# Optimization experiments

Measured on AMD Instinct MI355X. Metric: run time of the kernel, lower is better.

## Reference

```python
import jax, jax.numpy as jnp
import numpy as np

N, F, E, WID, M, K = 100000, 128, 128, 4, 25000, 16
HID = WID * F    # width * num_features = 512
DHID = WID * E   # discriminator hidden = 512
EPS = 1e-5


def _v2v(x, v_idx, w_e):
    """Hypergraph v2v mean aggregation: v->e mean (scaled by w_e), then e->v mean."""
    Mm, Kk = v_idx.shape
    C = x.shape[1]
    ef = jnp.zeros((Mm, C), x.dtype)
    for k in range(Kk):  # K is small and static; avoids a [M,K,C] materialization
        ef = ef + x[v_idx[:, k]]
    ef = ef * (w_e / Kk)[:, None]  # weighted edge features [M, C]
    out = jnp.zeros_like(x)
    deg = jnp.zeros((x.shape[0],), x.dtype)
    for k in range(Kk):
        out = out.at[v_idx[:, k]].add(ef)
        deg = deg.at[v_idx[:, k]].add(1.0)
    return out / jnp.maximum(deg, 1.0)[:, None]


def _bn(h, g, bt):
    # BatchNorm1d in training mode: biased batch stats over vertex dim
    m = h.mean(0)
    v = ((h - m) ** 2).mean(0)
    return g * (h - m) * jax.lax.rsqrt(v + EPS) + bt


def _conv(x, Wt, b, g, bt, v_idx, w_e, last=False):
    h = _bn(x @ Wt.T + b, g, bt)
    h = _v2v(h, v_idx, w_e)
    return h if last else jax.nn.relu(h)  # dropout = identity (eval mode)


def setup_inputs() -> dict:
    key = jax.random.key(0)
    ks = iter(jax.random.split(key, 64))

    def lin(o, i):
        s = 1.0 / np.sqrt(i)
        return (jax.random.uniform(next(ks), (o, i), minval=-s, maxval=s, dtype=jnp.float32),
                jax.random.uniform(next(ks), (o,), minval=-s, maxval=s, dtype=jnp.float32))

    d = {}
    d["X"] = jax.random.normal(next(ks), (N, F), dtype=jnp.float32)
    d["v_idx"] = jax.random.randint(next(ks), (M, K), 0, N, dtype=jnp.int32)
    d["w_e"] = jax.random.uniform(next(ks), (M,), dtype=jnp.float32)
    for name, (o, i) in [("enc1", (HID, F)), ("enc2", (E, HID)), ("fc", (E, HID)),
                         ("f1u", (E, E)), ("f2u", (E, E)), ("f1r", (E, E)), ("f2r", (E, E)),
                         ("f1", (E, E)), ("f2", (E, E)),
                         ("dis1", (DHID, E)), ("dis2", (2, DHID)),
                         ("dec1", (HID, E)), ("dec2", (F, HID))]:
        Wt, b = lin(o, i)
        d[name + "_W"] = Wt
        d[name + "_b"] = b
    for name, c in [("enc1", HID), ("enc2", E), ("dis1", DHID), ("dis2", 2), ("dec1", HID), ("dec2", F)]:
        d[name + "_g"] = jnp.ones((c,), jnp.float32)
        d[name + "_bt"] = jnp.zeros((c,), jnp.float32)
    return d


def reference(X, v_idx, w_e,
              enc1_W, enc1_b, enc2_W, enc2_b, fc_W, fc_b,
              f1u_W, f1u_b, f2u_W, f2u_b, f1r_W, f1r_b, f2r_W, f2r_b,
              f1_W, f1_b, f2_W, f2_b,
              dis1_W, dis1_b, dis2_W, dis2_b, dec1_W, dec1_b, dec2_W, dec2_b,
              enc1_g, enc1_bt, enc2_g, enc2_bt, dis1_g, dis1_bt, dis2_g, dis2_bt,
              dec1_g, dec1_bt, dec2_g, dec2_bt):
    # encoder (returns last output and first-layer output)
    x1 = _conv(X, enc1_W, enc1_b, enc1_g, enc1_bt, v_idx, w_e)            # [N, HID]
    xe = _conv(x1, enc2_W, enc2_b, enc2_g, enc2_bt, v_idx, w_e, last=True)  # [N, E]
    xe1 = x1 @ fc_W.T + fc_b                                               # [N, E]
    # GRU-style gating
    z = jax.nn.sigmoid(xe1 @ f1u_W.T + f1u_b + xe @ f2u_W.T + f2u_b)
    r = jax.nn.sigmoid(xe1 @ f1r_W.T + f1r_b + xe @ f2r_W.T + f2r_b)
    o = jnp.tanh(xe1 @ f1_W.T + f1_b + (r * xe) @ f2_W.T + f2_b)
    outs = z * o + (1.0 - z) * xe                                          # [N, E]
    # attention pooling (n = input_size - 1)
    dd = (outs - outs.mean(0)) ** 2
    vv = dd.sum(0) / (N - 1)
    ee = dd / (4.0 * (vv + 0.001)) + 0.5
    proto = (outs * jax.nn.sigmoid(ee)).sum(0)                             # [E]
    # gradient reversal is identity in the forward pass
    h = _conv(outs, dis1_W, dis1_b, dis1_g, dis1_bt, v_idx, w_e)
    xdis = _conv(h, dis2_W, dis2_b, dis2_g, dis2_bt, v_idx, w_e, last=True)  # [N, 2]
    h = _conv(outs, dec1_W, dec1_b, dec1_g, dec1_bt, v_idx, w_e)
    x_de = _conv(h, dec2_W, dec2_b, dec2_g, dec2_bt, v_idx, w_e, last=True)  # [N, F]
    return (outs, x_de, proto, xdis)
```

## Files before the change

### kernel.cpp

```cpp
#include <hip/hip_runtime.h>
#include <cstddef>
#include <cstdint>

static constexpr int NV = 100000;
static constexpr int NP = 100096;
static constexpr int ME = 25000;
static constexpr int MEP = 25088;
static constexpr int KE = 16;
static constexpr float BN_EPS = 1e-5f;

typedef unsigned int u32;
typedef __attribute__((ext_vector_type(8))) short s16x8;
typedef __attribute__((ext_vector_type(8))) unsigned short u16x8;
typedef __attribute__((ext_vector_type(4))) float f32x4;

__device__ __forceinline__ float sigm(float x) { return 1.0f / (1.0f + expf(-x)); }
__device__ __forceinline__ float bf2f(unsigned short u) {
    union { u32 i; float f; } v; v.i = ((u32)u) << 16; return v.f;
}
__device__ __forceinline__ unsigned short f2bf(float f) {
    union { float f; u32 i; } v; v.f = f;
    u32 u = v.i;
    return (unsigned short)((u + 0x7FFFu + ((u >> 16) & 1u)) >> 16);
}

#define GLD16(g, l) __builtin_amdgcn_global_load_lds(                          \
    (__attribute__((address_space(1))) const unsigned int*)(g),                \
    (__attribute__((address_space(3))) unsigned int*)(l), 16, 0, 0)

#define STAGE_A(b, k0)                                                         \
  {                                                                            \
    unsigned short* sA_ = sm + (b) * 8192;                                     \
    _Pragma("unroll")                                                          \
    for (int i_ = 0; i_ < 4; ++i_) {                                           \
      const unsigned short* g_ = A + (size_t)(bm + 32 * w + 8 * i_ + (l >> 3)) * IC + (k0) + swz; \
      GLD16(g_, sA_ + 2048 * w + 512 * i_);                                    \
    }                                                                          \
  }

__global__ __launch_bounds__(256)
void mfma_gemm(const unsigned short* __restrict__ A, int IC,
               const unsigned short* __restrict__ W, const float* __restrict__ bias,
               unsigned short* __restrict__ Cb, int ldb, int cb0,
               unsigned short* __restrict__ Cb2, int ldb2, int splitN,
               float* __restrict__ s1f, float* __restrict__ s2f, int statsC)
{
    __shared__ unsigned short sm[2 * 8192];
    const int bm = blockIdx.y * 128;
    const int bn = blockIdx.x * 64;
    const int tid = threadIdx.x;
    const int l = tid & 63, w = tid >> 6;
    const int wrow = w >> 1, wcol = w & 1;

    f32x4 acc[4][2];
    #pragma unroll
    for (int m = 0; m < 4; ++m)
        #pragma unroll
        for (int n = 0; n < 2; ++n)
            #pragma unroll
            for (int r = 0; r < 4; ++r) acc[m][n][r] = 0.f;

    const int swz = (((l & 7) ^ (l >> 3)) << 3);
    const int nt = IC >> 6;

    STAGE_A(0, 0);
    asm volatile("s_waitcnt vmcnt(0)" ::: "memory");
    __builtin_amdgcn_s_barrier();

    for (int t = 0; t < nt; ++t) {
        const int cur = t & 1;
        if (t + 1 < nt) STAGE_A(cur ^ 1, (t + 1) << 6);
        const unsigned short* sA = sm + cur * 8192;
        #pragma unroll
        for (int ks = 0; ks < 2; ++ks) {
            const int koff = ks * 32 + ((l >> 4) << 3);
            s16x8 afr[4], bfr[2];
            #pragma unroll
            for (int m = 0; m < 4; ++m) {
                int row = wrow * 64 + m * 16 + (l & 15);
                afr[m] = *(const s16x8*)&sA[row * 64 + (koff ^ ((l & 7) << 3))];
            }
            #pragma unroll
            for (int n = 0; n < 2; ++n) {
                int col = bn + wcol * 32 + n * 16 + (l & 15);
                bfr[n] = *(const s16x8*)&W[(size_t)col * IC + (t << 6) + koff];
            }
            #pragma unroll
            for (int m = 0; m < 4; ++m)
                #pragma unroll
                for (int n = 0; n < 2; ++n)
                    acc[m][n] = __builtin_amdgcn_mfma_f32_16x16x32_bf16(
                        afr[m], bfr[n], acc[m][n], 0, 0, 0);
        }
        asm volatile("s_waitcnt vmcnt(0)" ::: "memory");
        __builtin_amdgcn_s_barrier();
    }

    unsigned short* dst = Cb;
    int ld = ldb, co = cb0;
    if (Cb2 && bn >= splitN) { dst = Cb2; ld = ldb2; co = -splitN; }

    #pragma unroll
    for (int n = 0; n < 2; ++n) {
        const int col = bn + wcol * 32 + n * 16 + (l & 15);
        const float bs = bias[col];
        float ssum = 0.f, sq = 0.f;
        #pragma unroll
        for (int m = 0; m < 4; ++m) {
            const int row0 = bm + wrow * 64 + m * 16 + ((l >> 4) << 2);
            #pragma unroll
            for (int r = 0; r < 4; ++r) {
                float v = acc[m][n][r] + bs;
                int row = row0 + r;
                if (dst) dst[(size_t)row * ld + co + col] = f2bf(v);
                if (s1f && col < statsC && row < NV) { ssum += v; sq += v * v; }
            }
        }
        if (s1f && col < statsC) {
            ssum += __shfl_xor(ssum, 16); ssum += __shfl_xor(ssum, 32);
            sq   += __shfl_xor(sq, 16);   sq   += __shfl_xor(sq, 32);
            if ((l >> 4) == 0) {
                atomicAdd(&s1f[col], ssum);
                atomicAdd(&s2f[col], sq);
            }
        }
    }
}

__global__ __launch_bounds__(256)
void mfma_gemm_vtx2(const unsigned short* __restrict__ A,
                    const unsigned short* __restrict__ W,
                    const float* __restrict__ P, const float* __restrict__ Q,
                    const float* __restrict__ sw,
                    unsigned short* __restrict__ dst, int ldd, int colStart,
                    int disCols, const unsigned short* __restrict__ disW,
                    float2* __restrict__ pre22p)
{
    const int IC = 128;
    __shared__ unsigned short sm[2 * 8192];
    const int bm = blockIdx.y * 128;
    const int bx = blockIdx.x;
    const int bn0 = bx * 128;
    const int tid = threadIdx.x;
    const int l = tid & 63, w = tid >> 6;
    const int wrow = w >> 1, wcol = w & 1;

    f32x4 acc[4][4];
    #pragma unroll
    for (int m = 0; m < 4; ++m)
        #pragma unroll
        for (int n = 0; n < 4; ++n)
            #pragma unroll
            for (int r = 0; r < 4; ++r) acc[m][n][r] = 0.f;

    const int swz = (((l & 7) ^ (l >> 3)) << 3);

    STAGE_A(0, 0);
    asm volatile("s_waitcnt vmcnt(0)" ::: "memory");
    __builtin_amdgcn_s_barrier();

    #pragma unroll
    for (int t = 0; t < 2; ++t) {
        const int cur = t & 1;
        if (t == 0) STAGE_A(1, 64);
        const unsigned short* sA = sm + cur * 8192;
        #pragma unroll
        for (int ks = 0; ks < 2; ++ks) {
            const int koff = ks * 32 + ((l >> 4) << 3);
            s16x8 afr[4], bfr[4];
            #pragma unroll
            for (int m = 0; m < 4; ++m) {
                int row = wrow * 64 + m * 16 + (l & 15);
                afr[m] = *(const s16x8*)&sA[row * 64 + (koff ^ ((l & 7) << 3))];
            }
            #pragma unroll
            for (int n = 0; n < 4; ++n) {
                int colg = bn0 + wcol * 64 + n * 16 + (l & 15);
                bfr[n] = *(const s16x8*)&W[(size_t)colg * 128 + (t << 6) + koff];
            }
            #pragma unroll
            for (int m = 0; m < 4; ++m)
                #pragma unroll
                for (int n = 0; n < 4; ++n)
                    acc[m][n] = __builtin_amdgcn_mfma_f32_16x16x32_bf16(
                        afr[m], bfr[n], acc[m][n], 0, 0, 0);
        }
        asm volatile("s_waitcnt vmcnt(0)" ::: "memory");
        __builtin_amdgcn_s_barrier();
    }

    if (bn0 < disCols) {
        float pc[4], qc[4], w0f[4], w1f[4];
        #pragma unroll
        for (int n = 0; n < 4; ++n) {
            int colg = bn0 + wcol * 64 + n * 16 + (l & 15);
            pc[n] = P[colg]; qc[n] = Q[colg];
            w0f[n] = bf2f(disW[colg]);
            w1f[n] = bf2f(disW[512 + colg]);
        }
        const int slice = bx * 2 + wcol;
        #pragma unroll
        for (int m = 0; m < 4; ++m) {
            const int row0 = bm + wrow * 64 + m * 16 + ((l >> 4) << 2);
            #pragma unroll
            for (int r = 0; r < 4; ++r) {
                const int row = row0 + r;
                const float swr = sw[row];
                float p0 = 0.f, p1 = 0.f;
                #pragma unroll
                for (int n = 0; n < 4; ++n) {
                    float h = fmaxf(pc[n] * acc[m][n][r] + swr * qc[n], 0.f);
                    p0 += h * w0f[n];
                    p1 += h * w1f[n];
                }
                p0 += __shfl_xor(p0, 1); p0 += __shfl_xor(p0, 2);
                p0 += __shfl_xor(p0, 4); p0 += __shfl_xor(p0, 8);
                p1 += __shfl_xor(p1, 1); p1 += __shfl_xor(p1, 2);
                p1 += __shfl_xor(p1, 4); p1 += __shfl_xor(p1, 8);
                if ((l & 15) == 0)
                    pre22p[(size_t)slice * NP + row] = make_float2(p0, p1);
            }
        }
    } else {
        #pragma unroll
        for (int n = 0; n < 4; ++n) {
            const int colg = bn0 + wcol * 64 + n * 16 + (l & 15);
            const float pc = P[colg], qc = Q[colg];
            #pragma unroll
            for (int m = 0; m < 4; ++m) {
                const int row0 = bm + wrow * 64 + m * 16 + ((l >> 4) << 2);
                #pragma unroll
                for (int r = 0; r < 4; ++r) {
                    const int row = row0 + r;
                    float h = fmaxf(pc * acc[m][n][r] + sw[row] * qc, 0.f);
                    dst[(size_t)row * ldd + colg - colStart] = f2bf(h);
                }
            }
        }
    }
}

__global__ void reduce22(const float2* __restrict__ p, float* __restrict__ pre22)
{
    int v = blockIdx.x * 256 + threadIdx.x;
    if (v >= NV) return;
    float a = 0.f, b = 0.f;
    #pragma unroll
    for (int s = 0; s < 8; ++s) {
        float2 t = p[(size_t)s * NP + v];
        a += t.x; b += t.y;
    }
    pre22[2 * v] = a;
    pre22[2 * v + 1] = b;
}

__global__ __launch_bounds__(256)
void cov_kernel(const unsigned short* __restrict__ A, float* __restrict__ cov)
{
    __shared__ unsigned short T[128 * 64];
    const int tid = threadIdx.x;
    const int l = tid & 63, w = tid >> 6;

    f32x4 acc[2][8];
    #pragma unroll
    for (int m = 0; m < 2; ++m)
        #pragma unroll
        for (int n = 0; n < 8; ++n)
            #pragma unroll
            for (int r = 0; r < 4; ++r) acc[m][n][r] = 0.f;

    const int r0 = blockIdx.x * 1024;
    for (int ch = 0; ch < 16; ++ch) {
        const int rbase = r0 + ch * 64;
        __syncthreads();
        #pragma unroll
        for (int q = 0; q < 4; ++q) {
            int idx = tid + q * 256;
            int r = idx & 63, cg = idx >> 6;
            int row = rbase + r;
            u16x8 u = {0, 0, 0, 0, 0, 0, 0, 0};
            if (row < NV) u = *(const u16x8*)&A[(size_t)row * 128 + cg * 8];
            #pragma unroll
            for (int j = 0; j < 8; ++j) {
                int c = cg * 8 + j;
                T[c * 64 + (r ^ ((c & 7) << 3))] = u[j];
            }
        }
        __syncthreads();
        #pragma unroll
        for (int ks = 0; ks < 2; ++ks) {
            const int koff = ks * 32 + ((l >> 4) << 3);
            s16x8 fi[2], fj[8];
            #pragma unroll
            for (int m = 0; m < 2; ++m) {
                int c = (w * 2 + m) * 16 + (l & 15);
                fi[m] = *(const s16x8*)&T[c * 64 + (koff ^ ((c & 7) << 3))];
            }
            #pragma unroll
            for (int n = 0; n < 8; ++n) {
                int c = n * 16 + (l & 15);
                fj[n] = *(const s16x8*)&T[c * 64 + (koff ^ ((c & 7) << 3))];
            }
            #pragma unroll
            for (int m = 0; m < 2; ++m)
                #pragma unroll
                for (int n = 0; n < 8; ++n)
                    acc[m][n] = __builtin_amdgcn_mfma_f32_16x16x32_bf16(
                        fi[m], fj[n], acc[m][n], 0, 0, 0);
        }
    }
    #pragma unroll
    for (int m = 0; m < 2; ++m) {
        #pragma unroll
        for (int n = 0; n < 8; ++n) {
            #pragma unroll
            for (int r = 0; r < 4; ++r) {
                int row = (w * 2 + m) * 16 + ((l >> 4) << 2) + r;
                int col = n * 16 + (l & 15);
                atomicAdd(&cov[row * 128 + col], acc[m][n][r]);
            }
        }
    }
}

__global__ __launch_bounds__(128)
void quadform_kernel(const float* __restrict__ cov, const float* __restrict__ colsum,
                     const unsigned short* __restrict__ Wt, const float* __restrict__ bias,
                     float* __restrict__ s1, float* __restrict__ s2)
{
    const int c = blockIdx.x, i = threadIdx.x;
    __shared__ float wv[128];
    __shared__ float red[128][2];
    float wi = bf2f(Wt[c * 128 + i]);
    wv[i] = wi;
    __syncthreads();
    const float* crow = cov + i * 128;
    float dot = 0.f;
    #pragma unroll 8
    for (int j = 0; j < 128; ++j) dot += crow[j] * wv[j];
    red[i][0] = wi * dot;
    red[i][1] = wi * colsum[i];
    __syncthreads();
    for (int s = 64; s > 0; s >>= 1) {
        if (i < s) { red[i][0] += red[i + s][0]; red[i][1] += red[i + s][1]; }
        __syncthreads();
    }
    if (i == 0) {
        float b = bias[c];
        float ws = red[0][1];
        s1[c] = ws + (float)NV * b;
        s2[c] = red[0][0] + 2.f * b * ws + (float)NV * b * b;
    }
}

__global__ void prep_weights(const float* e1, const float* e2, const float* fcw,
                             const float* d1, const float* dc1, const float* dc2,
                             const float* ds2,
                             const float* f1u, const float* f2u,
                             const float* f1r, const float* f2r,
                             const float* f1, const float* f2,
                             const float* f1ub, const float* f2ub,
                             const float* f1rb, const float* f2rb,
                             const float* f1b, const float* f2b,
                             const float* ds1b, const float* dc1b,
                             const float* e2b, const float* fcb,
                             unsigned short* WB, float* bzr, float* bo,
                             float* bdd, float* bef)
{
    int i = blockIdx.x * 256 + threadIdx.x;
    if (i < 65536)           WB[i] = f2bf(e1[i]);
    else if (i < 131072)     WB[i] = f2bf(e2[i - 65536]);
    else if (i < 196608)     WB[i] = f2bf(fcw[i - 131072]);
    else if (i < 262144)     WB[i] = f2bf(d1[i - 196608]);
    else if (i < 327680)     WB[i] = f2bf(dc1[i - 262144]);
    else if (i < 393216)     WB[i] = f2bf(dc2[i - 327680]);
    else if (i < 394240)     WB[i] = f2bf(ds2[i - 393216]);
    else if (i < 459776) {
        int j = i - 394240, row = j >> 8, c = j & 255;
        float v;
        if (row < 128) v = (c < 128) ? f1u[row * 128 + c] : f2u[row * 128 + c - 128];
        else { int rr = row - 128; v = (c < 128) ? f1r[rr * 128 + c] : f2r[rr * 128 + c - 128]; }
        WB[i] = f2bf(v);
    } else if (i < 492544) {
        int j = i - 459776, row = j >> 8, c = j & 255;
        float v = (c < 128) ? f1[row * 128 + c] : f2[row * 128 + c - 128];
        WB[i] = f2bf(v);
    } else if (i < 492800) {
        int o = i - 492544;
        bzr[o] = (o < 128) ? (f1ub[o] + f2ub[o]) : (f1rb[o - 128] + f2rb[o - 128]);
    } else if (i < 492928) {
        int o = i - 492800;
        bo[o] = f1b[o] + f2b[o];
    } else if (i < 493952) {
        int o = i - 492928;
        bdd[o] = (o < 512) ? ds1b[o] : dc1b[o - 512];
    } else if (i < 494208) {
        int o = i - 493952;
        bef[o] = (o < 128) ? e2b[o] : fcb[o - 128];
    }
}

__global__ void cvt_f32_bf16(const float* __restrict__ in, unsigned short* __restrict__ out, int n)
{
    int i = (blockIdx.x * 256 + threadIdx.x) * 4;
    if (i < n) {
        float4 v = *reinterpret_cast<const float4*>(&in[i]);
        out[i] = f2bf(v.x); out[i + 1] = f2bf(v.y);
        out[i + 2] = f2bf(v.z); out[i + 3] = f2bf(v.w);
    }
}

__global__ void bn_finalize_kernel(const float* __restrict__ s1, const float* __restrict__ s2,
                                   const float* __restrict__ g, const float* __restrict__ bt,
                                   float* __restrict__ scale, float* __restrict__ shift,
                                   int C, float invN)
{
    int c = threadIdx.x;
    if (c < C) {
        float m = s1[c] * invN;
        float v = fmaxf(s2[c] * invN - m * m, 0.f);
        float sc = g[c] * rsqrtf(v + BN_EPS);
        scale[c] = sc;
        shift[c] = bt[c] - m * sc;
    }
}

__global__ void bn_finalize_pq(const float* __restrict__ s1, const float* __restrict__ s2,
                               const float* __restrict__ g, const float* __restrict__ bt,
                               const float* __restrict__ bias,
                               float* __restrict__ P, float* __restrict__ Q,
                               int C, int off, float invN)
{
    int c = threadIdx.x;
    if (c < C) {
        int cc = off + c;
        float m = s1[cc] * invN;
        float v = fmaxf(s2[cc] * invN - m * m, 0.f);
        float sc = g[c] * rsqrtf(v + BN_EPS);
        float sh = bt[c] - m * sc;
        P[cc] = sc;
        Q[cc] = sc * bias[c] + sh;
    }
}

__global__ __launch_bounds__(256)
void edge_gather_sum(const unsigned short* __restrict__ x, const int* __restrict__ vidx,
                     unsigned short* __restrict__ ge)
{
    const int e = blockIdx.x * 16 + (threadIdx.x >> 4);
    const int cp = (threadIdx.x & 15) << 3;
    if (e >= ME) return;
    float s[8] = {};
    const int* vi = vidx + e * KE;
    #pragma unroll
    for (int k = 0; k < KE; ++k) {
        int v = vi[k];
        u16x8 u = *(const u16x8*)&x[(size_t)v * 128 + cp];
        #pragma unroll
        for (int j = 0; j < 8; ++j) s[j] += bf2f(u[j]);
    }
    u16x8 o;
    #pragma unroll
    for (int j = 0; j < 8; ++j) o[j] = f2bf(s[j]);
    *(u16x8*)&ge[(size_t)e * 128 + cp] = o;
}

__global__ __launch_bounds__(256)
void csr_gather_g2(const unsigned short* __restrict__ ge, const float* __restrict__ we,
                   const int* __restrict__ rowptr, const int* __restrict__ csr,
                   unsigned short* __restrict__ g2, float* __restrict__ swv)
{
    const int v = blockIdx.x * 16 + (threadIdx.x >> 4);
    const int lg = threadIdx.x & 15;
    if (v >= NP) return;
    if (v >= NV) {
        u16x8 z = {0, 0, 0, 0, 0, 0, 0, 0};
        *(u16x8*)&g2[(size_t)v * 128 + lg * 8] = z;
        if (swv && lg == 0) swv[v] = 0.f;
        return;
    }
    const int s = rowptr[v], e = rowptr[v + 1];
    float a[8] = {};
    float ws = 0.f;
    for (int i = s; i < e; ++i) {
        int ed = csr[i];
        float wt = we[ed];
        ws += wt;
        u16x8 u = *(const u16x8*)&ge[(size_t)ed * 128 + lg * 8];
        #pragma unroll
        for (int j = 0; j < 8; ++j) a[j] = fmaf(wt, bf2f(u[j]), a[j]);
    }
    float inv = 1.0f / (float)max(e - s, 1);
    float invK = inv * (1.0f / KE);
    u16x8 o;
    #pragma unroll
    for (int j = 0; j < 8; ++j) o[j] = f2bf(a[j] * invK);
    *(u16x8*)&g2[(size_t)v * 128 + lg * 8] = o;
    if (swv && lg == 0) swv[v] = ws * inv;
}

__global__ __launch_bounds__(256)
void edge_gather_bf(const unsigned short* __restrict__ pre, const int* __restrict__ vidx,
                    const float* __restrict__ we, const float* __restrict__ scl,
                    const float* __restrict__ shf, unsigned short* __restrict__ ef, int C)
{
    const int tpe = C >> 3;
    const int epb = 256 / tpe;
    const int e = blockIdx.x * epb + threadIdx.x / tpe;
    const int cp = (threadIdx.x % tpe) << 3;
    if (e >= ME) return;
    float s[8] = {};
    const int* vi = vidx + e * KE;
    #pragma unroll
    for (int k = 0; k < KE; ++k) {
        int v = vi[k];
        u16x8 u = *(const u16x8*)&pre[(size_t)v * C + cp];
        #pragma unroll
        for (int j = 0; j < 8; ++j) s[j] += bf2f(u[j]);
    }
    float wv = we[e] * (1.0f / KE);
    u16x8 o;
    #pragma unroll
    for (int j = 0; j < 8; ++j)
        o[j] = f2bf(wv * (scl[cp + j] * s[j] + (float)KE * shf[cp + j]));
    *(u16x8*)&ef[(size_t)e * C + cp] = o;
}

__global__ void edge_gather2_kernel(const float* __restrict__ X, const int* __restrict__ vidx,
                                    const float* __restrict__ we, const float* __restrict__ scale,
                                    const float* __restrict__ shift, float* __restrict__ ef)
{
    int e = blockIdx.x * blockDim.x + threadIdx.x;
    if (e >= ME) return;
    float s0 = 0.f, s1v = 0.f;
    #pragma unroll
    for (int k = 0; k < KE; ++k) {
        int v = vidx[e * KE + k];
        s0 += X[2 * v];
        s1v += X[2 * v + 1];
    }
    float w = we[e] * (1.0f / KE);
    ef[2 * e]     = w * (scale[0] * s0 + (float)KE * shift[0]);
    ef[2 * e + 1] = w * (scale[1] * s1v + (float)KE * shift[1]);
}

__global__ void deg_kernel(const int* __restrict__ vidx, int* __restrict__ deg)
{
    int i = blockIdx.x * blockDim.x + threadIdx.x;
    if (i < ME * KE) atomicAdd(&deg[vidx[i]], 1);
}

__global__ void scan_block_kernel(const int* __restrict__ deg, int* __restrict__ rowptr,
                                  int* __restrict__ blocksums, int n)
{
    __shared__ int tmp[256];
    int i = blockIdx.x * 256 + threadIdx.x;
    int v = (i < n) ? deg[i] : 0;
    tmp[threadIdx.x] = v;
    __syncthreads();
    for (int off = 1; off < 256; off <<= 1) {
        int t = (threadIdx.x >= off) ? tmp[threadIdx.x - off] : 0;
        __syncthreads();
        tmp[threadIdx.x] += t;
        __syncthreads();
    }
    if (i < n) rowptr[i] = tmp[threadIdx.x] - v;
    if (threadIdx.x == 255) blocksums[blockIdx.x] = tmp[255];
}

__global__ void scan_sums_par(int* __restrict__ bs, int nb)
{
    __shared__ int tmp[512];
    int t = threadIdx.x;
    int v = (t < nb) ? bs[t] : 0;
    tmp[t] = v;
    __syncthreads();
    for (int off = 1; off < 512; off <<= 1) {
        int u = (t >= off) ? tmp[t - off] : 0;
        __syncthreads();
        tmp[t] += u;
        __syncthreads();
    }
    if (t < nb) bs[t] = tmp[t] - v;
}

__global__ void scan_add_kernel(int* __restrict__ rowptr, const int* __restrict__ blocksums, int n)
{
    int i = blockIdx.x * 256 + threadIdx.x;
    if (i < n) rowptr[i] += blocksums[blockIdx.x];
    if (i == 0) rowptr[n] = ME * KE;
}

__global__ void csr_fill_kernel(const int* __restrict__ vidx, int* __restrict__ cursor,
                                int* __restrict__ csr)
{
    int i = blockIdx.x * blockDim.x + threadIdx.x;
    if (i < ME * KE) {
        int v = vidx[i];
        int pos = atomicAdd(&cursor[v], 1);
        csr[pos] = i >> 4;
    }
}

__global__ __launch_bounds__(256)
void csr_gather_bf(const unsigned short* __restrict__ ef, int ldE, int cb0E,
                   const int* __restrict__ rowptr, const int* __restrict__ csr,
                   float* __restrict__ outf, int ldf,
                   unsigned short* __restrict__ outb, int ldb, int cb0,
                   unsigned short* __restrict__ outb2, int ldb2,
                   int C, int relu)
{
    const int lpv = C >> 3;
    const int vpb = 256 / lpv;
    const int v = blockIdx.x * vpb + threadIdx.x / lpv;
    const int lg = threadIdx.x % lpv;
    if (v >= NV) return;
    const int s = rowptr[v], e = rowptr[v + 1];
    float a[8] = {};
    int i = s;
    for (; i + 2 <= e; i += 2) {
        int e0 = csr[i], e1 = csr[i + 1];
        u16x8 u0 = *(const u16x8*)&ef[(size_t)e0 * ldE + cb0E + lg * 8];
        u16x8 u1 = *(const u16x8*)&ef[(size_t)e1 * ldE + cb0E + lg * 8];
        #pragma unroll
        for (int j = 0; j < 8; ++j) a[j] += bf2f(u0[j]) + bf2f(u1[j]);
    }
    if (i < e) {
        int e0 = csr[i];
        u16x8 u0 = *(const u16x8*)&ef[(size_t)e0 * ldE + cb0E + lg * 8];
        #pragma unroll
        for (int j = 0; j < 8; ++j) a[j] += bf2f(u0[j]);
    }
    float inv = 1.0f / (float)max(e - s, 1);
    #pragma unroll
    for (int j = 0; j < 8; ++j) {
        float x = a[j] * inv;
        if (relu) x = fmaxf(x, 0.f);
        a[j] = x;
    }
    if (outf) {
        float* p = outf + (size_t)v * ldf + lg * 8;
        #pragma unroll
        for (int j = 0; j < 8; ++j) p[j] = a[j];
    }
    if (outb) {
        u16x8 o;
        #pragma unroll
        for (int j = 0; j < 8; ++j) o[j] = f2bf(a[j]);
        *(u16x8*)&outb[(size_t)v * ldb + cb0 + lg * 8] = o;
    }
    if (outb2) {
        u16x8 o;
        #pragma unroll
        for (int j = 0; j < 8; ++j) o[j] = f2bf(a[j]);
        *(u16x8*)&outb2[(size_t)v * ldb2 + lg * 8] = o;
    }
}

__global__ void csr_gather2_kernel(const float* __restrict__ ef, const int* __restrict__ rowptr,
                                   const int* __restrict__ csr, float* __restrict__ outp)
{
    int v = blockIdx.x * blockDim.x + threadIdx.x;
    if (v >= NV) return;
    int s = rowptr[v], e = rowptr[v + 1];
    float a0 = 0.f, a1 = 0.f;
    for (int i = s; i < e; ++i) {
        int ed = csr[i];
        a0 += ef[2 * ed];
        a1 += ef[2 * ed + 1];
    }
    float inv = 1.0f / (float)max(e - s, 1);
    outp[2 * v]     = a0 * inv;
    outp[2 * v + 1] = a1 * inv;
}

__global__ __launch_bounds__(256)
void colstats_bf(const unsigned short* __restrict__ Xb,
                 float* __restrict__ s1, float* __restrict__ s2)
{
    const int t = threadIdx.x;
    const int cg = t & 15;
    const int rs = t >> 4;
    float s[8] = {}, q[8] = {};
    for (int r = blockIdx.x * 16 + rs; r < NV; r += 256 * 16) {
        u16x8 u = *(const u16x8*)&Xb[(size_t)r * 128 + cg * 8];
        #pragma unroll
        for (int j = 0; j < 8; ++j) {
            float v = bf2f(u[j]);
            s[j] += v; q[j] += v * v;
        }
    }
    __shared__ float ls[16][16][8];
    __shared__ float lq[16][16][8];
    #pragma unroll
    for (int j = 0; j < 8; ++j) { ls[rs][cg][j] = s[j]; lq[rs][cg][j] = q[j]; }
    __syncthreads();
    int c = t & 127;
    float a = 0.f;
    if (t < 128) {
        #pragma unroll
        for (int i = 0; i < 16; ++i) a += ls[i][c >> 3][c & 7];
        atomicAdd(&s1[c], a);
    } else {
        #pragma unroll
        for (int i = 0; i < 16; ++i) a += lq[i][c >> 3][c & 7];
        atomicAdd(&s2[c], a);
    }
}

__global__ void att_finalize_kernel(const float* __restrict__ s1, const float* __restrict__ s2,
                                    float* __restrict__ mu, float* __restrict__ qd, int C)
{
    int c = threadIdx.x;
    if (c < C) {
        float m = s1[c] / (float)NV;
        float vv = fmaxf((s2[c] - (float)NV * m * m) / (float)(NV - 1), 0.f);
        mu[c] = m;
        qd[c] = 1.0f / (4.0f * (vv + 0.001f));
    }
}

__global__ __launch_bounds__(256)
void proto_ws(const float* __restrict__ outsf, const float* __restrict__ mu,
              const float* __restrict__ qd, float* __restrict__ proto)
{
    const int t = threadIdx.x;
    const int cg = t & 31;
    const int rs = t >> 5;
    const float4* X4 = (const float4*)outsf;
    const float4 m = ((const float4*)mu)[cg];
    const float4 q = ((const float4*)qd)[cg];
    float4 acc = make_float4(0.f, 0.f, 0.f, 0.f);
    for (int r = blockIdx.x * 8 + rs; r < NV; r += 256 * 8) {
        float4 x = X4[(size_t)r * 32 + cg];
        float d0 = (x.x - m.x) * (x.x - m.x);
        float d1 = (x.y - m.y) * (x.y - m.y);
        float d2 = (x.z - m.z) * (x.z - m.z);
        float d3 = (x.w - m.w) * (x.w - m.w);
        acc.x += x.x * sigm(d0 * q.x + 0.5f);
        acc.y += x.y * sigm(d1 * q.y + 0.5f);
        acc.z += x.z * sigm(d2 * q.z + 0.5f);
        acc.w += x.w * sigm(d3 * q.w + 0.5f);
    }
    __shared__ float4 ls[8][32];
    ls[rs][cg] = acc;
    __syncthreads();
    if (t < 128) {
        float a = 0.f;
        #pragma unroll
        for (int i = 0; i < 8; ++i) {
            const float* f = (const float*)&ls[i][t >> 2];
            a += f[t & 3];
        }
        atomicAdd(&proto[t], a);
    }
}

__global__ void colstats2_kernel(const float* __restrict__ X, int N,
                                 float* __restrict__ s1, float* __restrict__ s2)
{
    __shared__ float red[256][4];
    int t = threadIdx.x;
    float a0 = 0, a1 = 0, b0 = 0, b1 = 0;
    for (int r = blockIdx.x * 256 + t; r < N; r += 256 * gridDim.x) {
        float x0 = X[2 * r], x1 = X[2 * r + 1];
        a0 += x0; b0 += x0 * x0;
        a1 += x1; b1 += x1 * x1;
    }
    red[t][0] = a0; red[t][1] = a1; red[t][2] = b0; red[t][3] = b1;
    __syncthreads();
    for (int s = 128; s > 0; s >>= 1) {
        if (t < s)
            for (int j = 0; j < 4; ++j) red[t][j] += red[t + s][j];
        __syncthreads();
    }
    if (t == 0) {
        atomicAdd(&s1[0], red[0][0]);
        atomicAdd(&s1[1], red[0][1]);
        atomicAdd(&s2[0], red[0][2]);
        atomicAdd(&s2[1], red[0][3]);
    }
}

__global__ void rx_kernel(const unsigned short* __restrict__ ZR, const unsigned short* __restrict__ xeb,
                          unsigned short* __restrict__ G, int n8)
{
    int idx = blockIdx.x * blockDim.x + threadIdx.x;
    if (idx >= n8) return;
    int i8 = idx * 8;
    int row = i8 >> 7, c = i8 & 127;
    u16x8 rv = *(const u16x8*)&ZR[(size_t)row * 256 + 128 + c];
    u16x8 xv = *(const u16x8*)&xeb[i8];
    u16x8 g;
    #pragma unroll
    for (int j = 0; j < 8; ++j)
        g[j] = f2bf(sigm(bf2f(rv[j])) * bf2f(xv[j]));
    *(u16x8*)&G[(size_t)row * 256 + 128 + c] = g;
}

__global__ void gru_out_kernel(const unsigned short* __restrict__ ZR, const unsigned short* __restrict__ Opre,
                               const unsigned short* __restrict__ xeb,
                               float* __restrict__ outs, unsigned short* __restrict__ outsb,
                               float* __restrict__ outsf, int n8)
{
    int idx = blockIdx.x * blockDim.x + threadIdx.x;
    if (idx >= n8) return;
    int i8 = idx * 8;
    int row = i8 >> 7, c = i8 & 127;
    u16x8 zv = *(const u16x8*)&ZR[(size_t)row * 256 + c];
    u16x8 ov = *(const u16x8*)&Opre[i8];
    u16x8 xv = *(const u16x8*)&xeb[i8];
    float val[8];
    u16x8 ob;
    #pragma unroll
    for (int j = 0; j < 8; ++j) {
        float z = sigm(bf2f(zv[j]));
        float o = tanhf(bf2f(ov[j]));
        float xe = bf2f(xv[j]);
        val[j] = z * o + (1.f - z) * xe;
        ob[j] = f2bf(val[j]);
    }
    *(float4*)&outs[i8]     = make_float4(val[0], val[1], val[2], val[3]);
    *(float4*)&outs[i8 + 4] = make_float4(val[4], val[5], val[6], val[7]);
    *(float4*)&outsf[i8]     = make_float4(val[0], val[1], val[2], val[3]);
    *(float4*)&outsf[i8 + 4] = make_float4(val[4], val[5], val[6], val[7]);
    *(u16x8*)&outsb[i8] = ob;
}

extern "C" void kernel_launch(void* const* d_in, const int* in_sizes, int n_in,
                              void* d_out, int out_size, void* d_ws, size_t ws_size,
                              hipStream_t stream)
{
    const float* X      = (const float*)d_in[0];
    const int*   vidx   = (const int*)  d_in[1];
    const float* we     = (const float*)d_in[2];
    const float* enc1_W = (const float*)d_in[3];  const float* enc1_b = (const float*)d_in[4];
    const float* enc2_W = (const float*)d_in[5];  const float* enc2_b = (const float*)d_in[6];
    const float* fc_W   = (const float*)d_in[7];  const float* fc_b   = (const float*)d_in[8];
    const float* f1u_W  = (const float*)d_in[9];  const float* f1u_b  = (const float*)d_in[10];
    const float* f2u_W  = (const float*)d_in[11]; const float* f2u_b  = (const float*)d_in[12];
    const float* f1r_W  = (const float*)d_in[13]; const float* f1r_b  = (const float*)d_in[14];
    const float* f2r_W  = (const float*)d_in[15]; const float* f2r_b  = (const float*)d_in[16];
    const float* f1_W   = (const float*)d_in[17]; const float* f1_b   = (const float*)d_in[18];
    const float* f2_W   = (const float*)d_in[19]; const float* f2_b   = (const float*)d_in[20];
    const float* dis1_W = (const float*)d_in[21]; const float* dis1_b = (const float*)d_in[22];
    const float* dis2_W = (const float*)d_in[23]; const float* dis2_b = (const float*)d_in[24];
    const float* dec1_W = (const float*)d_in[25]; const float* dec1_b = (const float*)d_in[26];
    const float* dec2_W = (const float*)d_in[27]; const float* dec2_b = (const float*)d_in[28];
    const float* enc1_g = (const float*)d_in[29]; const float* enc1_bt = (const float*)d_in[30];
    const float* enc2_g = (const float*)d_in[31]; const float* enc2_bt = (const float*)d_in[32];
    const float* dis1_g = (const float*)d_in[33]; const float* dis1_bt = (const float*)d_in[34];
    const float* dis2_g = (const float*)d_in[35]; const float* dis2_bt = (const float*)d_in[36];
    const float* dec1_g = (const float*)d_in[37]; const float* dec1_bt = (const float*)d_in[38];
    const float* dec2_g = (const float*)d_in[39]; const float* dec2_bt = (const float*)d_in[40];

    float* out   = (float*)d_out;
    float* outs  = out;
    float* x_de  = out + 12800000;
    float* proto = out + 25600000;
    float* xdis  = out + 25600128;

    char* base = (char*)d_ws;
    unsigned short* bufA = (unsigned short*)base;
    char* p = base + (size_t)NP * 512 * 2;
    unsigned short* bufE = (unsigned short*)p; p += (size_t)MEP * 1024 * 2;
    unsigned short* Greg = (unsigned short*)p;
    unsigned short* Xbf  = Greg;
    unsigned short* outsb = Greg + (size_t)NP * 128;
    p += (size_t)NP * 256 * 2;
    unsigned short* x1bf = (unsigned short*)p; p += (size_t)NP * 512 * 2;
    unsigned short* WB = (unsigned short*)p; p += 492544 * 2 + 1024;
    float* bzr = (float*)p; p += 256 * 4;
    float* bo  = (float*)p; p += 128 * 4;
    float* bdd = (float*)p; p += 1024 * 4;
    float* bef = (float*)p; p += 256 * 4;
    float* s1  = (float*)p; p += 1024 * 4;
    float* s2  = (float*)p; p += 1024 * 4;
    float* scl = (float*)p; p += 1024 * 4;
    float* shf = (float*)p; p += 1024 * 4;
    float* sX1 = (float*)p; p += 128 * 4;
    float* sX2 = (float*)p; p += 128 * 4;
    float* sA1 = (float*)p; p += 128 * 4;
    float* sA2 = (float*)p; p += 128 * 4;
    float* covX = (float*)p; p += 16384 * 4;
    float* covA = (float*)p; p += 16384 * 4;
    int* deg    = (int*)p; p += (size_t)NV * 4;
    int* rowptr = (int*)p; p += (size_t)(NV + 1) * 4;
    int* cursor = (int*)p; p += (size_t)NV * 4;
    int* bsums  = (int*)p; p += 512 * 4;
    int* csr    = (int*)p; p += (size_t)ME * KE * 4;
    float* outsf = (float*)p; p += (size_t)NP * 128 * 4;
    unsigned short* ge = (unsigned short*)p; p += (size_t)MEP * 128 * 2;
    float* sw = (float*)p;

    unsigned short* g2 = bufE + (size_t)MEP * 128;
    float2* pre22p = (float2*)(bufE + (size_t)MEP * 128 + (size_t)NP * 128);

    unsigned short* pre128 = bufA;
    unsigned short* xe_bf  = bufA + (size_t)NP * 128;
    unsigned short* ZR     = bufA + (size_t)NP * 256;
    unsigned short* Opre   = bufA;
    unsigned short* hdec   = bufA;
    float* pre22 = (float*)(Greg + (size_t)NP * 128);
    float* bufEf = (float*)bufE;

    unsigned short* wenc1 = WB;
    unsigned short* wenc2 = WB + 65536;
    unsigned short* wdd   = WB + 196608;
    unsigned short* wdec2 = WB + 327680;
    unsigned short* wdis2 = WB + 393216;
    unsigned short* wzr   = WB + 394240;
    unsigned short* wo    = WB + 459776;

    const int n128 = NV * 128;
    const int n8 = n128 / 8;
    const int nScanBlocks = (NV + 255) / 256;

    auto gemm = [&](const unsigned short* A, int ic, const unsigned short* W, const float* b,
                    unsigned short* Cb, int ldb, int cb0,
                    unsigned short* Cb2, int ldb2, int splitN,
                    int oc, float* st1, float* st2, int statsC) {
        dim3 g(oc / 64, NP / 128);
        mfma_gemm<<<g, 256, 0, stream>>>(A, ic, W, b, Cb, ldb, cb0, Cb2, ldb2, splitN,
                                         st1, st2, statsC);
    };

    prep_weights<<<1931, 256, 0, stream>>>(enc1_W, enc2_W, fc_W, dis1_W, dec1_W, dec2_W, dis2_W,
                                           f1u_W, f2u_W, f1r_W, f2r_W, f1_W, f2_W,
                                           f1u_b, f2u_b, f1r_b, f2r_b, f1_b, f2_b,
                                           dis1_b, dec1_b, enc2_b, fc_b,
                                           WB, bzr, bo, bdd, bef);
    cvt_f32_bf16<<<(n128 / 4 + 255) / 256, 256, 0, stream>>>(X, Xbf, n128);

    hipMemsetAsync(deg, 0, NV * sizeof(int), stream);
    deg_kernel<<<(ME * KE + 255) / 256, 256, 0, stream>>>(vidx, deg);
    scan_block_kernel<<<nScanBlocks, 256, 0, stream>>>(deg, rowptr, bsums, NV);
    scan_sums_par<<<1, 512, 0, stream>>>(bsums, nScanBlocks);
    scan_add_kernel<<<nScanBlocks, 256, 0, stream>>>(rowptr, bsums, NV);
    hipMemcpyAsync(cursor, rowptr, NV * sizeof(int), hipMemcpyDeviceToDevice, stream);
    csr_fill_kernel<<<(ME * KE + 255) / 256, 256, 0, stream>>>(vidx, cursor, csr);

    hipMemsetAsync(sX1, 0, 256 * sizeof(float), stream);
    hipMemsetAsync(covX, 0, 16384 * sizeof(float), stream);
    colstats_bf<<<256, 256, 0, stream>>>(Xbf, sX1, sX2);
    cov_kernel<<<98, 256, 0, stream>>>(Xbf, covX);
    quadform_kernel<<<512, 128, 0, stream>>>(covX, sX1, wenc1, enc1_b, s1, s2);
    bn_finalize_pq<<<1, 512, 0, stream>>>(s1, s2, enc1_g, enc1_bt, enc1_b, scl, shf, 512, 0, 1.0f / NV);
    edge_gather_sum<<<(ME + 15) / 16, 256, 0, stream>>>(Xbf, vidx, ge);
    csr_gather_g2<<<NP / 16, 256, 0, stream>>>(ge, we, rowptr, csr, g2, sw);
    { dim3 g(4, NP / 128);
      mfma_gemm_vtx2<<<g, 256, 0, stream>>>(g2, wenc1, scl, shf, sw, x1bf, 512, 0,
                                            0, nullptr, nullptr); }

    hipMemsetAsync(s1, 0, 2048 * sizeof(float), stream);
    gemm(x1bf, 512, wenc2, bef, pre128, 128, 0, Greg, 256, 128, 256, s1, s2, 128);
    bn_finalize_kernel<<<1, 512, 0, stream>>>(s1, s2, enc2_g, enc2_bt, scl, shf, 128, 1.0f / NV);
    edge_gather_bf<<<(ME + 15) / 16, 256, 0, stream>>>(pre128, vidx, we, scl, shf, bufE, 128);
    csr_gather_bf<<<NV / 16, 256, 0, stream>>>(bufE, 128, 0, rowptr, csr,
        nullptr, 0, Greg, 256, 128, xe_bf, 128, 128, 0);

    gemm(Greg, 256, wzr, bzr, ZR, 256, 0, nullptr, 0, 1 << 30, 256, nullptr, nullptr, 0);
    rx_kernel<<<(n8 + 255) / 256, 256, 0, stream>>>(ZR, xe_bf, Greg, n8);
    gemm(Greg, 256, wo, bo, Opre, 128, 0, nullptr, 0, 1 << 30, 128, nullptr, nullptr, 0);
    gru_out_kernel<<<(n8 + 255) / 256, 256, 0, stream>>>(ZR, Opre, xe_bf, outs, outsb, outsf, n8);

    hipMemsetAsync(sA1, 0, 256 * sizeof(float), stream);
    colstats_bf<<<256, 256, 0, stream>>>(outsb, sA1, sA2);
    att_finalize_kernel<<<1, 128, 0, stream>>>(sA1, sA2, scl, shf, 128);
    hipMemsetAsync(proto, 0, 128 * sizeof(float), stream);
    proto_ws<<<256, 256, 0, stream>>>(outsf, scl, shf, proto);

    hipMemsetAsync(covA, 0, 16384 * sizeof(float), stream);
    cov_kernel<<<98, 256, 0, stream>>>(outsb, covA);
    quadform_kernel<<<1024, 128, 0, stream>>>(covA, sA1, wdd, bdd, s1, s2);
    bn_finalize_pq<<<1, 512, 0, stream>>>(s1, s2, dis1_g, dis1_bt, dis1_b, scl, shf, 512, 0, 1.0f / NV);
    bn_finalize_pq<<<1, 512, 0, stream>>>(s1, s2, dec1_g, dec1_bt, dec1_b, scl, shf, 512, 512, 1.0f / NV);
    edge_gather_sum<<<(ME + 15) / 16, 256, 0, stream>>>(outsb, vidx, ge);
    csr_gather_g2<<<NP / 16, 256, 0, stream>>>(ge, we, rowptr, csr, g2, nullptr);
    { dim3 g(8, NP / 128);
      mfma_gemm_vtx2<<<g, 256, 0, stream>>>(g2, wdd, scl, shf, sw, hdec, 512, 512,
                                            512, wdis2, pre22p); }
    reduce22<<<(NV + 255) / 256, 256, 0, stream>>>(pre22p, pre22);

    hipMemsetAsync(s1, 0, 2048 * sizeof(float), stream);
    colstats2_kernel<<<64, 256, 0, stream>>>(pre22, NV, s1, s2);
    bn_finalize_kernel<<<1, 512, 0, stream>>>(s1, s2, dis2_g, dis2_bt, scl, shf, 2, 1.0f / NV);
    edge_gather2_kernel<<<(ME + 255) / 256, 256, 0, stream>>>(pre22, vidx, we, scl, shf, bufEf);
    csr_gather2_kernel<<<(NV + 255) / 256, 256, 0, stream>>>(bufEf, rowptr, csr, xdis);

    hipMemsetAsync(s1, 0, 2048 * sizeof(float), stream);
    gemm(hdec, 512, wdec2, dec2_b, Greg, 128, 0, nullptr, 0, 1 << 30, 128, s1, s2, 128);
    bn_finalize_kernel<<<1, 512, 0, stream>>>(s1, s2, dec2_g, dec2_bt, scl, shf, 128, 1.0f / NV);
    edge_gather_bf<<<(ME + 15) / 16, 256, 0, stream>>>(Greg, vidx, we, scl, shf, bufE, 128);
    csr_gather_bf<<<NV / 16, 256, 0, stream>>>(bufE, 128, 0, rowptr, csr,
        x_de, 128, nullptr, 0, 0, nullptr, 0, 128, 0);
}
```

Before: 906.3 us.

## Stage full A row tiles in LDS and loop over all output column blocks

Replaces the vertex GEMM kernel with one that loads a complete 128x128 A tile into LDS once. It then iterates over all output column blocks within the same workgroup, processing two row tiles per block and prefetching the second. The goal is to remove the redundant re-reads of the A matrix across column-block workgroups. In exchange, the grid shrinks substantially, per-block work becomes serial, and doubling LDS usage can reduce occupancy.

```diff
diff --git a/kernel.cpp b/kernel.cpp
--- a/kernel.cpp
+++ b/kernel.cpp
@@ -36,6 +36,18 @@
       const unsigned short* g_ = A + (size_t)(bm + 32 * w + 8 * i_ + (l >> 3)) * IC + (k0) + swz; \
       GLD16(g_, sA_ + 2048 * w + 512 * i_);                                    \
     }                                                                          \
+  }
+
+#define STAGE_FULL(b, bmv)                                                     \
+  {                                                                            \
+    unsigned short* sD_ = sm + (b) * 16384;                                    \
+    _Pragma("unroll")                                                          \
+    for (int kh_ = 0; kh_ < 2; ++kh_)                                          \
+      _Pragma("unroll")                                                        \
+      for (int i_ = 0; i_ < 4; ++i_) {                                         \
+        const unsigned short* g_ = A + (size_t)((bmv) + 32 * w + 8 * i_ + (l >> 3)) * 128 + kh_ * 64 + swz; \
+        GLD16(g_, sD_ + kh_ * 8192 + (32 * w + 8 * i_) * 64);                  \
+      }                                                                        \
   }
 
 __global__ __launch_bounds__(256)
@@ -128,115 +140,119 @@
 }
 
 __global__ __launch_bounds__(256)
-void mfma_gemm_vtx2(const unsigned short* __restrict__ A,
+void mfma_gemm_vtx3(const unsigned short* __restrict__ A,
                     const unsigned short* __restrict__ W,
                     const float* __restrict__ P, const float* __restrict__ Q,
                     const float* __restrict__ sw,
                     unsigned short* __restrict__ dst, int ldd, int colStart,
-                    int disCols, const unsigned short* __restrict__ disW,
+                    int OCB, int disCols, const unsigned short* __restrict__ disW,
                     float2* __restrict__ pre22p)
 {
-    const int IC = 128;
-    __shared__ unsigned short sm[2 * 8192];
-    const int bm = blockIdx.y * 128;
-    const int bx = blockIdx.x;
-    const int bn0 = bx * 128;
+    __shared__ unsigned short sm[2 * 16384];
     const int tid = threadIdx.x;
     const int l = tid & 63, w = tid >> 6;
     const int wrow = w >> 1, wcol = w & 1;
-
-    f32x4 acc[4][4];
-    #pragma unroll
-    for (int m = 0; m < 4; ++m)
-        #pragma unroll
-        for (int n = 0; n < 4; ++n)
-            #pragma unroll
-            for (int r = 0; r < 4; ++r) acc[m][n][r] = 0.f;
-
     const int swz = (((l & 7) ^ (l >> 3)) << 3);
 
-    STAGE_A(0, 0);
+    const int rt0 = blockIdx.y * 2;
+
+    STAGE_FULL(0, rt0 * 128);
     asm volatile("s_waitcnt vmcnt(0)" ::: "memory");
     __builtin_amdgcn_s_barrier();
 
     #pragma unroll
-    for (int t = 0; t < 2; ++t) {
-        const int cur = t & 1;
-        if (t == 0) STAGE_A(1, 64);
-        const unsigned short* sA = sm + cur * 8192;
-        #pragma unroll
-        for (int ks = 0; ks < 2; ++ks) {
-            const int koff = ks * 32 + ((l >> 4) << 3);
-            s16x8 afr[4], bfr[4];
-            #pragma unroll
-            for (int m = 0; m < 4; ++m) {
-                int row = wrow * 64 + m * 16 + (l & 15);
-                afr[m] = *(const s16x8*)&sA[row * 64 + (koff ^ ((l & 7) << 3))];
-            }
-            #pragma unroll
-            for (int n = 0; n < 4; ++n) {
-                int colg = bn0 + wcol * 64 + n * 16 + (l & 15);
-                bfr[n] = *(const s16x8*)&W[(size_t)colg * 128 + (t << 6) + koff];
-            }
+    for (int rti = 0; rti < 2; ++rti) {
+        const int cur = rti;
+        const int bmv = (rt0 + rti) * 128;
+        if (rti == 0) STAGE_FULL(1, bmv + 128);
+
+        for (int cb = 0; cb < OCB; ++cb) {
+            f32x4 acc[4][4];
             #pragma unroll
             for (int m = 0; m < 4; ++m)
                 #pragma unroll
                 for (int n = 0; n < 4; ++n)
-                    acc[m][n] = __builtin_amdgcn_mfma_f32_16x16x32_bf16(
-                        afr[m], bfr[n], acc[m][n], 0, 0, 0);
+                    #pragma unroll
+                    for (int r = 0; r < 4; ++r) acc[m][n][r] = 0.f;
+
+            #pragma unroll
+            for (int kh = 0; kh < 2; ++kh) {
+                const unsigned short* sA = sm + cur * 16384 + kh * 8192;
+                #pragma unroll
+                for (int ks = 0; ks < 2; ++ks) {
+                    const int koff = ks * 32 + ((l >> 4) << 3);
+                    s16x8 afr[4], bfr[4];
+                    #pragma unroll
+                    for (int m = 0; m < 4; ++m) {
+                        int row = wrow * 64 + m * 16 + (l & 15);
+                        afr[m] = *(const s16x8*)&sA[row * 64 + (koff ^ ((l & 7) << 3))];
+                    }
+                    #pragma unroll
+                    for (int n = 0; n < 4; ++n) {
+                        int colg = cb * 128 + wcol * 64 + n * 16 + (l & 15);
+                        bfr[n] = *(const s16x8*)&W[(size_t)colg * 128 + kh * 64 + koff];
+                    }
+                    #pragma unroll
+                    for (int m = 0; m < 4; ++m)
+                        #pragma unroll
+                        for (int n = 0; n < 4; ++n)
+                            acc[m][n] = __builtin_amdgcn_mfma_f32_16x16x32_bf16(
+                                afr[m], bfr[n], acc[m][n], 0, 0, 0);
+                }
+            }
+
+            if (cb * 128 < disCols) {
+                float pc[4], qc[4], w0f[4], w1f[4];
+                #pragma unroll
+                for (int n = 0; n < 4; ++n) {
+                    int colg = cb * 128 + wcol * 64 + n * 16 + (l & 15);
+                    pc[n] = P[colg]; qc[n] = Q[colg];
+                    w0f[n] = bf2f(disW[colg]);
+                    w1f[n] = bf2f(disW[512 + colg]);
+                }
+                const int slice = cb * 2 + wcol;
+                #pragma unroll
+                for (int m = 0; m < 4; ++m) {
+                    const int row0 = bmv + wrow * 64 + m * 16 + ((l >> 4) << 2);
+                    #pragma unroll
+                    for (int r = 0; r < 4; ++r) {
+                        const int row = row0 + r;
+                        const float swr = sw[row];
+                        float p0 = 0.f, p1 = 0.f;
+                        #pragma unroll
+                        for (int n = 0; n < 4; ++n) {
+                            float h = fmaxf(pc[n] * acc[m][n][r] + swr * qc[n], 0.f);
+                            p0 += h * w0f[n];
+                            p1 += h * w1f[n];
+                        }
+                        p0 += __shfl_xor(p0, 1); p0 += __shfl_xor(p0, 2);
+                        p0 += __shfl_xor(p0, 4); p0 += __shfl_xor(p0, 8);
+                        p1 += __shfl_xor(p1, 1); p1 += __shfl_xor(p1, 2);
+                        p1 += __shfl_xor(p1, 4); p1 += __shfl_xor(p1, 8);
+                        if ((l & 15) == 0)
+                            pre22p[(size_t)slice * NP + row] = make_float2(p0, p1);
+                    }
+                }
+            } else {
+                #pragma unroll
+                for (int n = 0; n < 4; ++n) {
+                    const int colg = cb * 128 + wcol * 64 + n * 16 + (l & 15);
+                    const float pc = P[colg], qc = Q[colg];
+                    #pragma unroll
+                    for (int m = 0; m < 4; ++m) {
+                        const int row0 = bmv + wrow * 64 + m * 16 + ((l >> 4) << 2);
+                        #pragma unroll
+                        for (int r = 0; r < 4; ++r) {
+                            const int row = row0 + r;
+                            float h = fmaxf(pc * acc[m][n][r] + sw[row] * qc, 0.f);
+                            dst[(size_t)row * ldd + colg - colStart] = f2bf(h);
+                        }
+                    }
+                }
+            }
         }
         asm volatile("s_waitcnt vmcnt(0)" ::: "memory");
         __builtin_amdgcn_s_barrier();
-    }
-
-    if (bn0 < disCols) {
-        float pc[4], qc[4], w0f[4], w1f[4];
-        #pragma unroll
-        for (int n = 0; n < 4; ++n) {
-            int colg = bn0 + wcol * 64 + n * 16 + (l & 15);
-            pc[n] = P[colg]; qc[n] = Q[colg];
-            w0f[n] = bf2f(disW[colg]);
-            w1f[n] = bf2f(disW[512 + colg]);
-        }
-        const int slice = bx * 2 + wcol;
-        #pragma unroll
-        for (int m = 0; m < 4; ++m) {
-            const int row0 = bm + wrow * 64 + m * 16 + ((l >> 4) << 2);
-            #pragma unroll
-            for (int r = 0; r < 4; ++r) {
-                const int row = row0 + r;
-                const float swr = sw[row];
-                float p0 = 0.f, p1 = 0.f;
-                #pragma unroll
-                for (int n = 0; n < 4; ++n) {
-                    float h = fmaxf(pc[n] * acc[m][n][r] + swr * qc[n], 0.f);
-                    p0 += h * w0f[n];
-                    p1 += h * w1f[n];
-                }
-                p0 += __shfl_xor(p0, 1); p0 += __shfl_xor(p0, 2);
-                p0 += __shfl_xor(p0, 4); p0 += __shfl_xor(p0, 8);
-                p1 += __shfl_xor(p1, 1); p1 += __shfl_xor(p1, 2);
-                p1 += __shfl_xor(p1, 4); p1 += __shfl_xor(p1, 8);
-                if ((l & 15) == 0)
-                    pre22p[(size_t)slice * NP + row] = make_float2(p0, p1);
-            }
-        }
-    } else {
-        #pragma unroll
-        for (int n = 0; n < 4; ++n) {
-            const int colg = bn0 + wcol * 64 + n * 16 + (l & 15);
-            const float pc = P[colg], qc = Q[colg];
-            #pragma unroll
-            for (int m = 0; m < 4; ++m) {
-                const int row0 = bm + wrow * 64 + m * 16 + ((l >> 4) << 2);
-                #pragma unroll
-                for (int r = 0; r < 4; ++r) {
-                    const int row = row0 + r;
-                    float h = fmaxf(pc * acc[m][n][r] + sw[row] * qc, 0.f);
-                    dst[(size_t)row * ldd + colg - colStart] = f2bf(h);
-                }
-            }
-        }
     }
 }
 
@@ -948,9 +964,9 @@
     bn_finalize_pq<<<1, 512, 0, stream>>>(s1, s2, enc1_g, enc1_bt, enc1_b, scl, shf, 512, 0, 1.0f / NV);
     edge_gather_sum<<<(ME + 15) / 16, 256, 0, stream>>>(Xbf, vidx, ge);
     csr_gather_g2<<<NP / 16, 256, 0, stream>>>(ge, we, rowptr, csr, g2, sw);
-    { dim3 g(4, NP / 128);
-      mfma_gemm_vtx2<<<g, 256, 0, stream>>>(g2, wenc1, scl, shf, sw, x1bf, 512, 0,
-                                            0, nullptr, nullptr); }
+    { dim3 g(1, NP / 256);
+      mfma_gemm_vtx3<<<g, 256, 0, stream>>>(g2, wenc1, scl, shf, sw, x1bf, 512, 0,
+                                            4, 0, nullptr, nullptr); }
 
     hipMemsetAsync(s1, 0, 2048 * sizeof(float), stream);
     gemm(x1bf, 512, wenc2, bef, pre128, 128, 0, Greg, 256, 128, 256, s1, s2, 128);
@@ -977,9 +993,9 @@
     bn_finalize_pq<<<1, 512, 0, stream>>>(s1, s2, dec1_g, dec1_bt, dec1_b, scl, shf, 512, 512, 1.0f / NV);
     edge_gather_sum<<<(ME + 15) / 16, 256, 0, stream>>>(outsb, vidx, ge);
     csr_gather_g2<<<NP / 16, 256, 0, stream>>>(ge, we, rowptr, csr, g2, nullptr);
-    { dim3 g(8, NP / 128);
-      mfma_gemm_vtx2<<<g, 256, 0, stream>>>(g2, wdd, scl, shf, sw, hdec, 512, 512,
-                                            512, wdis2, pre22p); }
+    { dim3 g(1, NP / 256);
+      mfma_gemm_vtx3<<<g, 256, 0, stream>>>(g2, wdd, scl, shf, sw, hdec, 512, 512,
+                                            8, 512, wdis2, pre22p); }
     reduce22<<<(NV + 255) / 256, 256, 0, stream>>>(pre22p, pre22);
 
     hipMemsetAsync(s1, 0, 2048 * sizeof(float), stream);
```

Result: slower. 977.1 us (+7.8%).
